# Kernel tuning notes

Hardware: AMD Instinct MI355X
Metric: run time of the kernel (lower is better)

The kernel has to match this reference:

```python
import jax, jax.numpy as jnp
import numpy as np

# ---- static config (matches init_kwargs: nlevs=[2,3,4], Pyr_mode=1, dfilt='pkva') ----
NLEVS = (2, 3, 4)
L = 3
# symmetric length-12 ladder (lifting) filter in the spirit of the 'pkva' ladder filter
_PKVA_HALF = np.array([0.6300, -0.1930, 0.0972, -0.0526, 0.0272, -0.0144])
PKVA = np.concatenate([_PKVA_HALF[::-1], _PKVA_HALF])


def _lp_hp_masks(H, W):
    """Meyer-style smooth lowpass/highpass frequency masks (rcos smooth_func)."""
    def phi(n):
        w = np.abs(2.0 * np.pi * np.fft.fftfreq(n))
        s = np.clip((w - np.pi / 3.0) / (np.pi / 3.0), 0.0, 1.0)
        beta = s ** 4 * (35.0 - 84.0 * s + 70.0 * s ** 2 - 20.0 * s ** 3)
        return np.cos(0.5 * np.pi * beta)
    Lm = phi(H)[:, None] * phi(W)[None, :]
    Hm = np.sqrt(np.clip(1.0 - Lm ** 2, 0.0, None))
    return jnp.asarray(Lm, jnp.float32), jnp.asarray(Hm, jnp.float32)


def _pyr_dec(x, nlev):
    """PyrNDDEC_mm, Pyr_mode=1: FFT-domain smooth LP/HP split, dyadic decimation of LP."""
    bands = []
    for _ in range(nlev):
        H, W = x.shape[-2], x.shape[-1]
        Lm, Hm = _lp_hp_masks(H, W)
        Xf = jnp.fft.fft2(x)
        bands.append(jnp.fft.ifft2(Xf * Hm).real.astype(x.dtype))
        x = jnp.fft.ifft2(Xf * Lm).real.astype(x.dtype)[..., ::2, ::2]
    return [x] + bands[::-1]  # y[0]=coarsest lowpass, y[1..L]=bandpass coarse->fine


def _conv1d_wrap(x, f, axis):
    """1D circular ('wrap') convolution along `axis`."""
    K = f.shape[0]
    x = jnp.moveaxis(x, axis, -1)
    pad = [(0, 0)] * (x.ndim - 1) + [(K // 2, K - 1 - K // 2)]
    xp = jnp.pad(x, pad, mode='wrap')
    shp = xp.shape
    y = jax.lax.conv_general_dilated(xp.reshape(-1, 1, shp[-1]),
                                     f.reshape(1, 1, K).astype(x.dtype), (1,), 'VALID')
    y = y.reshape(shp[:-1] + (shp[-1] - K + 1,))
    return jnp.moveaxis(y, -1, axis)


def _fan_split(x, axis, f):
    """One ladder-structured fan filter-bank stage with quincunx coset split."""
    other = -2 if axis == -1 else -1
    n_other = x.shape[other]
    shape = [1] * x.ndim
    shape[other] = n_other
    idx = jnp.arange(n_other)
    # fan <-> diamond modulation along the other axis
    sign = (1 - 2 * (idx % 2)).astype(x.dtype).reshape(shape)
    xm = x * sign
    # quincunx cosets: shift odd lines by 1 along split axis, then deinterleave
    parity = ((idx % 2) == 1).reshape(shape)
    xs = jnp.where(parity, jnp.roll(xm, -1, axis=axis), xm)
    if axis == -1:
        p0, p1 = xs[..., 0::2], xs[..., 1::2]
    else:
        p0, p1 = xs[..., 0::2, :], xs[..., 1::2, :]
    # ladder (lifting) predict/update with 1D filter f
    d = p1 - _conv1d_wrap(p0, f, axis)
    s = p0 + 0.5 * _conv1d_wrap(d, f, axis)
    return s, d


def _dfbdec(x, f, n):
    """n-level directional filter bank (ladder structure). Returns (2^n, ...) stack."""
    subs = x[None]  # (M, B, 1, H, W), all subbands same shape per level -> vectorized
    axis = -1
    for _ in range(n):
        s, d = _fan_split(subs, axis, f)
        subs = jnp.concatenate([s, d], axis=0)
        axis = -2 if axis == -1 else -1
    return subs


def setup_inputs() -> dict:
    key = jax.random.key(0)
    x = jax.random.normal(key, (16, 1, 1024, 1024), dtype=jnp.float32)
    return {"x": x}


def reference(x):
    f = jnp.asarray(PKVA, x.dtype)
    y = _pyr_dec(x, L)
    outs = [y[0]]  # coarsest lowpass (B,1,128,128)
    for k in range(1, L + 1):
        outs.append(_dfbdec(y[k], f, NLEVS[k - 1]))
    # (lowpass, 4 dirs @128x128, 8 dirs @(256,128), 16 dirs @(256,256))
    return tuple(outs)
```

## Files before the change

### kernel.cpp

```cpp
#include <hip/hip_runtime.h>
#include <math.h>

#define PI_F 3.14159265358979323846f

__constant__ float c_pkva[12] = {
  -0.0144f, 0.0272f, -0.0526f, 0.0972f, -0.193f, 0.63f,
   0.63f, -0.193f, 0.0972f, -0.0526f, 0.0272f, -0.0144f
};

constexpr int ilog2c(int n) { int l = 0; while (n > 1) { n >>= 1; ++l; } return l; }

__device__ float g_phi[1920];
__device__ float2 g_tw[512];
constexpr int phi_off(int N) {
  return (N == 1024) ? 0 : (N == 512) ? 1024 : (N == 256) ? 1536 : 1792;
}

__device__ __forceinline__ float phi_dev(int k, int n) {
  int kk = (k < n - k) ? k : (n - k);
  float w = 2.0f * PI_F * (float)kk / (float)n;
  float s = (w - PI_F / 3.0f) * (3.0f / PI_F);
  s = fminf(fmaxf(s, 0.0f), 1.0f);
  float s2 = s * s;
  float beta = s2 * s2 * (35.0f - 84.0f * s + 70.0f * s2 - 20.0f * s2 * s);
  return __cosf(0.5f * PI_F * beta);
}

__global__ void phi_init_k() {
  int i = blockIdx.x * 256 + threadIdx.x;
  if (i < 1024)      g_phi[i] = phi_dev(i, 1024);
  else if (i < 1536) g_phi[i] = phi_dev(i - 1024, 512);
  else if (i < 1792) g_phi[i] = phi_dev(i - 1536, 256);
  else if (i < 1920) g_phi[i] = phi_dev(i - 1792, 128);
  else {
    int idx = i - 1920;
    if (idx >= 1 && idx < 512) {
      int l = 31 - __clz(idx);
      int Ns = 1 << l;
      float th = 2.0f * PI_F * (float)(idx - Ns) / (float)(4 * Ns);
      g_tw[idx] = make_float2(cosf(th), sinf(th));
    }
  }
}

__device__ __forceinline__ float2 cmul(float2 a, float2 b) {
  return make_float2(a.x * b.x - a.y * b.y, a.x * b.y + a.y * b.x);
}
__device__ __forceinline__ float2 cadd(float2 a, float2 b) { return make_float2(a.x + b.x, a.y + b.y); }
__device__ __forceinline__ float2 csub(float2 a, float2 b) { return make_float2(a.x - b.x, a.y - b.y); }

template <int N>
__device__ __forceinline__ int fft_core4(float2 (*sbuf)[N], float dirsign, int tid, int cur) {
  constexpr int LOG2 = ilog2c(N);
  constexpr int NT = N / 4;
  constexpr bool LEAD2 = (LOG2 & 1);
  if constexpr (LEAD2) {
#pragma unroll
    for (int j = tid; j < N / 2; j += NT) {
      float2 v0 = sbuf[cur][j], v1 = sbuf[cur][j + N / 2];
      float2 e = cadd(v0, v1), o = csub(v0, v1);
      *(float4*)&sbuf[cur ^ 1][2 * j] = make_float4(e.x, e.y, o.x, o.y);
    }
    cur ^= 1;
    __syncthreads();
  }
#pragma unroll
  for (int Ns = LEAD2 ? 2 : 1; Ns < N; Ns <<= 2) {
    int j = tid;
    int base = j & (Ns - 1);
    float2 t = g_tw[Ns + base];
    float2 w1 = make_float2(t.x, dirsign * t.y);
    float2 w2 = cmul(w1, w1);
    float2 w3 = cmul(w2, w1);
    float2 v0 = sbuf[cur][j];
    float2 v1 = cmul(sbuf[cur][j + N / 4], w1);
    float2 v2 = cmul(sbuf[cur][j + N / 2], w2);
    float2 v3 = cmul(sbuf[cur][j + 3 * (N / 4)], w3);
    float2 a0 = cadd(v0, v2), a1 = csub(v0, v2);
    float2 a2 = cadd(v1, v3), a3 = csub(v1, v3);
    float2 r1 = make_float2(-dirsign * a3.y, dirsign * a3.x);
    int idxD = ((j - base) << 2) + base;
    cur ^= 1;
    sbuf[cur][idxD]          = cadd(a0, a2);
    sbuf[cur][idxD + Ns]     = cadd(a1, r1);
    sbuf[cur][idxD + 2 * Ns] = csub(a0, a2);
    sbuf[cur][idxD + 3 * Ns] = csub(a1, r1);
    __syncthreads();
  }
  return cur;
}

template <int N, int LMODE, int SMODE>
__global__ void __launch_bounds__(N / 4)
fft_rows_k(const void* __restrict__ vin, void* __restrict__ vout,
           float dirsign, float scale) {
  constexpr int NT = N / 4;
  __shared__ __align__(16) float2 sbuf[2][N];
  const int tid = threadIdx.x;
  const int row = blockIdx.x;
  const int r = row & (N - 1);

  if (LMODE == 1) {
    const float2* in = (const float2*)vin;
#pragma unroll
    for (int i = tid; i < N; i += NT) {
      float2 v = in[(size_t)row * N + i];
      sbuf[0][i] = make_float2(v.x * scale, v.y * scale);
    }
  } else {
    const float2* in = (const float2*)vin;
    float pr = g_phi[phi_off(N) + r];
#pragma unroll
    for (int i = tid; i < N; i += NT) {
      float lm = pr * g_phi[phi_off(N) + i];
      float m = sqrtf(fmaxf(1.0f - lm * lm, 0.0f)) * scale;
      float2 v = in[(size_t)row * N + i];
      sbuf[0][i] = make_float2(v.x * m, v.y * m);
    }
  }
  __syncthreads();

  int cur = fft_core4<N>(sbuf, dirsign, tid, 0);

  if (SMODE == 0) {
    float2* outp = (float2*)vout;
#pragma unroll
    for (int i = tid; i < N; i += NT)
      outp[(size_t)row * N + i] = sbuf[cur][i];
  } else {
    float* outp = (float*)vout;
#pragma unroll
    for (int i = tid; i < N; i += NT)
      outp[(size_t)row * N + i] = sbuf[cur][i].x;
  }
}

template <int N, int LMODE>
__global__ void __launch_bounds__(N / 4)
fft_rows_cm_k(const float2* __restrict__ in, float2* __restrict__ outcm,
              float scale) {
  constexpr int NT = N / 4;
  __shared__ __align__(16) float2 sbuf[2][N];
  const int tid = threadIdx.x;
  const int img = blockIdx.y;
  const int b = blockIdx.x;
  const int q = ((b & 7) << (ilog2c(N) - 4)) + (b >> 3);
  float2 r0v[4], r1v[4];

#pragma unroll
  for (int half = 0; half < 2; ++half) {
    const int r = 2 * q + half;
    if constexpr (LMODE == 1) {
      const float2* rp = in + ((size_t)img * N + r) * N;
#pragma unroll
      for (int i = tid; i < N; i += NT) {
        float2 v = rp[i];
        sbuf[0][i] = make_float2(v.x * scale, v.y * scale);
      }
    } else if constexpr (LMODE == 2) {
      const float2* rp = in + ((size_t)img * N + r) * N;
      float pr = g_phi[phi_off(N) + r];
#pragma unroll
      for (int i = tid; i < N; i += NT) {
        float lm = pr * g_phi[phi_off(N) + i];
        float m = sqrtf(fmaxf(1.0f - lm * lm, 0.0f)) * scale;
        float2 v = rp[i];
        sbuf[0][i] = make_float2(v.x * m, v.y * m);
      }
    } else {
      const float2* fb = in + (size_t)img * (513 * 512);
      const float2* fr0 = fb + (size_t)r * 512;
      const float2* fr1 = fb + (size_t)(512 - r) * 512;
      float pr = g_phi[phi_off(512) + r];
#pragma unroll
      for (int i = tid; i < N; i += NT) {
        float2 a = fr0[i], bb = fr1[(512 - i) & 511];
        float lm = pr * g_phi[phi_off(512) + i];
        float m = sqrtf(fmaxf(1.0f - lm * lm, 0.0f)) * scale;
        sbuf[0][i] = make_float2((a.x + bb.x) * m, (a.y - bb.y) * m);
      }
    }
    __syncthreads();

    int cur = fft_core4<N>(sbuf, 1.0f, tid, 0);

#pragma unroll
    for (int i = tid, k = 0; i < N; i += NT, ++k) {
      float2 v = sbuf[cur][i];
      if (half == 0) r0v[k] = v; else r1v[k] = v;
    }
    __syncthreads();
  }

  float2* ob = outcm + (size_t)img * N * N + 2 * q;
#pragma unroll
  for (int i = tid, k = 0; i < N; i += NT, ++k)
    *(float4*)&ob[(size_t)i * N] = make_float4(r0v[k].x, r0v[k].y, r1v[k].x, r1v[k].y);
}

template <int N, int PITCH>
__global__ void __launch_bounds__(N / 4)
rfft_pairs_cm_k(const float* __restrict__ in, float2* __restrict__ out) {
  constexpr int NT = N / 4;
  __shared__ __align__(16) float2 sbuf[2][N];
  const int tid = threadIdx.x;
  const int img = blockIdx.x >> (ilog2c(N) - 1);
  const int b = blockIdx.x & (N / 2 - 1);
  const int r = ((b & 7) << (ilog2c(N) - 4)) + (b >> 3);
  const float* p0 = in + ((size_t)img * N + 2 * r) * N;
  const float* p1 = p0 + N;

#pragma unroll
  for (int i = tid; i < N; i += NT)
    sbuf[0][i] = make_float2(p0[i], p1[i]);
  __syncthreads();

  int cur = fft_core4<N>(sbuf, -1.0f, tid, 0);

  float2* ob = out + (size_t)img * ((size_t)PITCH * N) + 2 * r;
#pragma unroll
  for (int i = tid; i <= N / 2; i += NT) {
    float2 Z = sbuf[cur][i];
    float2 Zr = sbuf[cur][(N - i) & (N - 1)];
    float2 Zc = make_float2(Zr.x, -Zr.y);
    float2 o0 = make_float2(0.5f * (Z.x + Zc.x), 0.5f * (Z.y + Zc.y));
    float2 dd = make_float2(Z.x - Zc.x, Z.y - Zc.y);
    float2 o1 = make_float2(0.5f * dd.y, -0.5f * dd.x);
    *(float4*)&ob[(size_t)i * N] = make_float4(o0.x, o0.y, o1.x, o1.y);
  }
}

__global__ void transpose_rect_k(const float2* __restrict__ in,
                                 float2* __restrict__ out, int R, int C) {
  __shared__ float2 tile[32][33];
  int img = blockIdx.z;
  size_t base = (size_t)img * R * C;
  int c = blockIdx.x * 32 + threadIdx.x;
  int r0 = blockIdx.y * 32;
  for (int j = threadIdx.y; j < 32; j += 8)
    tile[j][threadIdx.x] = in[base + (size_t)(r0 + j) * C + c];
  __syncthreads();
  int r = blockIdx.y * 32 + threadIdx.x;
  int c0 = blockIdx.x * 32;
  for (int j = threadIdx.y; j < 32; j += 8)
    out[base + (size_t)(c0 + j) * R + r] = tile[threadIdx.x][j];
}

template <int N, int PITCH>
__global__ void __launch_bounds__(N / 4)
fft_col_half_k(float2* __restrict__ inout, float2* __restrict__ foldb) {
  constexpr int NT = N / 4;
  constexpr int NH = N / 2;
  __shared__ __align__(16) float2 sbuf[2][N];
  const int tid = threadIdx.x;
  const int kx = blockIdx.x;
  const int img = blockIdx.y;
  float2* rowp = inout + ((size_t)img * PITCH + kx) * N;

#pragma unroll
  for (int i = tid; i < N; i += NT)
    sbuf[0][i] = rowp[i];
  __syncthreads();

  int cur = fft_core4<N>(sbuf, -1.0f, tid, 0);

  const float pr = g_phi[phi_off(N) + kx];
  const float inv = 1.0f / (float)N;
  float2* fp = foldb + ((size_t)img * (NH + 1) + kx) * NH;
#pragma unroll
  for (int i = tid; i < NH; i += NT) {
    float2 vA = sbuf[cur][i];
    float2 vB = sbuf[cur][i + NH];
    float lmA = pr * g_phi[phi_off(N) + i];
    float lmB = pr * g_phi[phi_off(N) + i + NH];
    fp[i] = make_float2(0.25f * (vA.x * lmA + vB.x * lmB),
                        0.25f * (vA.y * lmA + vB.y * lmB));
    float hmA = sqrtf(fmaxf(1.0f - lmA * lmA, 0.0f)) * inv;
    float hmB = sqrtf(fmaxf(1.0f - lmB * lmB, 0.0f)) * inv;
    sbuf[cur][i]      = make_float2(vA.x * hmA, vA.y * hmA);
    sbuf[cur][i + NH] = make_float2(vB.x * hmB, vB.y * hmB);
  }
  __syncthreads();

  cur = fft_core4<N>(sbuf, 1.0f, tid, cur);

#pragma unroll
  for (int i = tid; i < N; i += NT)
    rowp[i] = sbuf[cur][i];
}

__global__ void __launch_bounds__(256)
fold_spec3_k(const float2* __restrict__ fold, float2* __restrict__ spec3) {
  __shared__ float2 s2a[512], s2b[512];
  const int rp = blockIdx.x;
  const int img = blockIdx.y;
  const float2* fb = fold + (size_t)img * (513 * 512);
  const float2* fr0 = fb + (size_t)rp * 512;
  const float2* fr1 = fb + (size_t)(512 - rp) * 512;
  const float2* fr2 = fb + (size_t)(rp + 256) * 512;
  const float2* fr3 = fb + (size_t)(256 - rp) * 512;
  for (int c = threadIdx.x; c < 512; c += 256) {
    int mc = (512 - c) & 511;
    float2 a0 = fr0[c], b0 = fr1[mc];
    float2 a1 = fr2[c], b1 = fr3[mc];
    s2a[c] = make_float2(a0.x + b0.x, a0.y - b0.y);
    s2b[c] = make_float2(a1.x + b1.x, a1.y - b1.y);
  }
  __syncthreads();
  float pr0 = g_phi[phi_off(512) + rp], pr1 = g_phi[phi_off(512) + rp + 256];
  float2* sp3 = spec3 + ((size_t)img << 16) + ((size_t)rp << 8);
  {
    int c = threadIdx.x;
    float pc0 = g_phi[phi_off(512) + c], pc1 = g_phi[phi_off(512) + c + 256];
    float2 v00 = s2a[c], v01 = s2a[c + 256], v10 = s2b[c], v11 = s2b[c + 256];
    float m00 = pr0 * pc0, m01 = pr0 * pc1, m10 = pr1 * pc0, m11 = pr1 * pc1;
    sp3[c] = make_float2(
        0.25f * (v00.x * m00 + v01.x * m01 + v10.x * m10 + v11.x * m11),
        0.25f * (v00.y * m00 + v01.y * m01 + v10.y * m10 + v11.y * m11));
  }
}

template <int N, int PITCH>
__global__ void __launch_bounds__(N / 4)
ifft_fan_pair_k(const float2* __restrict__ in, float* __restrict__ outb,
                float scale, int halfT) {
  constexpr int NT = N / 4;
  constexpr int W2 = N / 2;
  __shared__ __align__(16) float2 sbuf[2][N];
  const int tid = threadIdx.x;
  const int img = blockIdx.x >> (ilog2c(N) - 1);
  const int q = blockIdx.x & (N / 2 - 1);
  const int y0 = 2 * q;
  const float2* inA = in + ((size_t)img * N + y0) * PITCH;
  const float2* inB = inA + PITCH;

#pragma unroll
  for (int i = tid; i <= W2; i += NT) {
    float2 a = inA[i], b = inB[i];
    sbuf[0][i] = make_float2((a.x - b.y) * scale, (a.y + b.x) * scale);
  }
#pragma unroll
  for (int i = tid; i < W2 - 1; i += NT) {
    int m = W2 - 1 - i;
    float2 a = inA[m], b = inB[m];
    sbuf[0][W2 + 1 + i] = make_float2((a.x + b.y) * scale, (b.x - a.y) * scale);
  }
  __syncthreads();

  int cur = fft_core4<N>(sbuf, 1.0f, tid, 0);

  float* scratch = (float*)sbuf[cur ^ 1];
  float* xe = scratch;
  float* xo = scratch + W2;
  float* db = scratch + 2 * W2;
  const size_t rbase = ((size_t)img * N + y0) * W2;

  for (int sub = 0; sub < 2; ++sub) {
    const int par = sub;
    const float sgn = par ? -1.0f : 1.0f;
#pragma unroll
    for (int i = tid; i < N; i += NT) {
      float v = par ? sbuf[cur][i].y : sbuf[cur][i].x;
      int ii = (i - par) & (N - 1);
      if (ii & 1) xo[ii >> 1] = v; else xe[ii >> 1] = v;
    }
    __syncthreads();

    float* outs = outb + rbase + (size_t)sub * W2;
    float* outd = outb + halfT + rbase + (size_t)sub * W2;
#pragma unroll 2
    for (int j = tid; j < W2; j += NT) {
      float acc = 0.0f;
#pragma unroll
      for (int k = 0; k < 12; k++)
        acc += c_pkva[k] * xe[(j - 6 + k + W2) & (W2 - 1)];
      float dv = sgn * (xo[j] - acc);
      db[j] = dv;
      outd[j] = dv;
    }
    __syncthreads();
#pragma unroll 2
    for (int j = tid; j < W2; j += NT) {
      float acc = 0.0f;
#pragma unroll
      for (int k = 0; k < 12; k++)
        acc += c_pkva[k] * db[(j - 6 + k + W2) & (W2 - 1)];
      outs[j] = sgn * xe[j] + 0.5f * acc;
    }
    __syncthreads();
  }
}

template <int N>
__global__ void __launch_bounds__(N / 4)
ifft_fan_k(const float2* __restrict__ in, float* __restrict__ outb,
           float scale, int halfT) {
  constexpr int NT = N / 4;
  constexpr int W2 = N / 2;
  __shared__ __align__(16) float2 sbuf[2][N];
  const int tid = threadIdx.x;
  const int nr = blockIdx.x;
  const int r = nr & (N - 1);
  const int par = r & 1;
  const float sgn = par ? -1.0f : 1.0f;

#pragma unroll
  for (int i = tid; i < N; i += NT) {
    float2 v = in[(size_t)nr * N + i];
    sbuf[0][i] = make_float2(v.x * scale, v.y * scale);
  }
  __syncthreads();

  int cur = fft_core4<N>(sbuf, 1.0f, tid, 0);

  float* scratch = (float*)sbuf[cur ^ 1];
  float* xe = scratch;
  float* xo = scratch + W2;
  float* db = scratch + 2 * W2;
#pragma unroll
  for (int i = tid; i < N; i += NT) {
    float v = sbuf[cur][i].x;
    int ii = (i - par) & (N - 1);
    if (ii & 1) xo[ii >> 1] = v; else xe[ii >> 1] = v;
  }
  __syncthreads();

  float* outs = outb + (size_t)nr * W2;
  float* outd = outb + halfT + (size_t)nr * W2;
#pragma unroll 2
  for (int j = tid; j < W2; j += NT) {
    float acc = 0.0f;
#pragma unroll
    for (int k = 0; k < 12; k++)
      acc += c_pkva[k] * xe[(j - 6 + k + W2) & (W2 - 1)];
    float dv = sgn * (xo[j] - acc);
    db[j] = dv;
    outd[j] = dv;
  }
  __syncthreads();
#pragma unroll 2
  for (int j = tid; j < W2; j += NT) {
    float acc = 0.0f;
#pragma unroll
    for (int k = 0; k < 12; k++)
      acc += c_pkva[k] * db[(j - 6 + k + W2) & (W2 - 1)];
    outs[j] = sgn * xe[j] + 0.5f * acc;
  }
}

__global__ void alias_k(const float2* __restrict__ in, float2* __restrict__ out,
                        int N, int lgN2, int phiOff) {
  int idx = blockIdx.x * 256 + threadIdx.x;
  int N2 = N >> 1;
  int c = idx & (N2 - 1);
  int r = (idx >> lgN2) & (N2 - 1);
  int img = idx >> (2 * lgN2);
  float pr0 = g_phi[phiOff + r], pr1 = g_phi[phiOff + r + N2];
  float pc0 = g_phi[phiOff + c], pc1 = g_phi[phiOff + c + N2];
  size_t base = (size_t)img * N * N;
  float2 v00 = in[base + (size_t)r * N + c];
  float2 v01 = in[base + (size_t)r * N + c + N2];
  float2 v10 = in[base + (size_t)(r + N2) * N + c];
  float2 v11 = in[base + (size_t)(r + N2) * N + c + N2];
  float m00 = pr0 * pc0, m01 = pr0 * pc1, m10 = pr1 * pc0, m11 = pr1 * pc1;
  float2 o;
  o.x = 0.25f * (v00.x * m00 + v01.x * m01 + v10.x * m10 + v11.x * m11);
  o.y = 0.25f * (v00.y * m00 + v01.y * m01 + v10.y * m10 + v11.y * m11);
  out[((size_t)img << (2 * lgN2)) + ((size_t)r << lgN2) + c] = o;
}

__global__ void __launch_bounds__(256)
fs_row_k(const float* __restrict__ x, float* __restrict__ outb,
         int lgH, int lgW, int halfT) {
  __shared__ float xe[512], xo[512], db[512];
  int H = 1 << lgH, W = 1 << lgW, W2 = W >> 1;
  int nr = blockIdx.x;
  int r = nr & (H - 1);
  int par = r & 1;
  float sgn = par ? -1.0f : 1.0f;
  const float* xrow = x + (size_t)nr * W;
  for (int j = threadIdx.x; j < W2; j += 256) {
    xe[j] = sgn * xrow[(2 * j + par) & (W - 1)];
    xo[j] = sgn * xrow[(2 * j + 1 + par) & (W - 1)];
  }
  __syncthreads();
  float* outs = outb + (size_t)nr * W2;
  float* outd = outb + halfT + (size_t)nr * W2;
  for (int j = threadIdx.x; j < W2; j += 256) {
    float acc = 0.0f;
#pragma unroll
    for (int k = 0; k < 12; k++)
      acc += c_pkva[k] * xe[(j - 6 + k + W2) & (W2 - 1)];
    float dv = xo[j] - acc;
    db[j] = dv;
    outd[j] = dv;
  }
  __syncthreads();
  for (int j = threadIdx.x; j < W2; j += 256) {
    float acc = 0.0f;
#pragma unroll
    for (int k = 0; k < 12; k++)
      acc += c_pkva[k] * db[(j - 6 + k + W2) & (W2 - 1)];
    outs[j] = xe[j] + 0.5f * acc;
  }
}

template <int TI, int TC>
__global__ void __launch_bounds__(256)
fs_col_fused_k(const float* __restrict__ x, float* __restrict__ outb,
               int lgH, int lgW, int halfT) {
  constexpr int RE = 2 * TI + 48;
  constexpr int DE = TI + 12;
  constexpr int NR = 256 / TC;
  __shared__ float raw[RE][TC];
  __shared__ float dvs[DE][TC];
  const int H = 1 << lgH, W = 1 << lgW;
  const int c0 = blockIdx.x * TC;
  const int i0 = blockIdx.y * TI;
  const int n = blockIdx.z;
  const int tc = threadIdx.x & (TC - 1);
  const int tr = threadIdx.x / TC;
  const float* xim = x + ((size_t)n << (lgH + lgW));
  const int rbase = 2 * i0 - 24;
#pragma unroll
  for (int r = tr; r < RE; r += NR) {
    int rr = (rbase + r) & (H - 1);
    raw[r][tc] = xim[((size_t)rr << lgW) + c0 + tc];
  }
  __syncthreads();
  const int par = tc & 1;
  for (int j = tr; j < DE; j += NR) {
    float acc = 0.0f;
#pragma unroll
    for (int k = 0; k < 12; k++)
      acc += c_pkva[k] * raw[2 * j + 2 * k + par][tc];
    dvs[j][tc] = raw[2 * j + 13 + par][tc] - acc;
  }
  __syncthreads();
  const float sgn = par ? -1.0f : 1.0f;
  float* outs = outb + (((size_t)n << (lgH - 1)) << lgW);
  float* outd = outs + halfT;
  for (int i = tr; i < TI; i += NR) {
    float acc = 0.0f;
#pragma unroll
    for (int k = 0; k < 12; k++)
      acc += c_pkva[k] * dvs[i + k][tc];
    float p0v = raw[2 * i + 24 + par][tc];
    size_t off = ((size_t)(i0 + i) << lgW) + c0 + tc;
    outd[off] = sgn * dvs[i + 6][tc];
    outs[off] = sgn * (p0v + 0.5f * acc);
  }
}

__global__ void fill_err_k(float* out) {
  out[threadIdx.x] = 1.0e9f;
}

extern "C" void kernel_launch(void* const* d_in, const int* in_sizes, int n_in,
                              void* d_out, int out_size, void* d_ws, size_t ws_size,
                              hipStream_t stream) {
  const float* x = (const float*)d_in[0];
  float* out = (float*)d_out;
  char* ws = (char*)d_ws;

  const size_t NEED = 220266496ull;
  if (ws_size < NEED) {
    fill_err_k<<<dim3(1), dim3(256), 0, stream>>>(out);
    return;
  }

  float2* bufA  = (float2*)(ws);
  float2* bufB  = (float2*)(ws + 71303168);
  float2* foldb = (float2*)(ws + 142606336);
  float2* spec3 = (float2*)(ws + 209780736);
  float2* spec4 = (float2*)(ws + 218169344);

  float* out0 = out;
  float* out1 = out + 262144;
  float* out2 = out + 1310720;
  float* out3 = out + 5505024;

  phi_init_k<<<dim3(10), dim3(256), 0, stream>>>();

  rfft_pairs_cm_k<1024, 544><<<dim3(8192), dim3(256), 0, stream>>>(x, bufB);
  fft_col_half_k<1024, 544><<<dim3(513, 16), dim3(256), 0, stream>>>(bufB, foldb);
  fold_spec3_k<<<dim3(256, 16), dim3(256), 0, stream>>>(foldb, spec3);
  transpose_rect_k<<<dim3(32, 17, 16), dim3(32, 8), 0, stream>>>(bufB, bufA, 544, 1024);
  ifft_fan_pair_k<1024, 544><<<dim3(8192), dim3(256), 0, stream>>>(bufA, (float*)bufB, 1.0f / 1024.0f, 8388608);
  fs_col_fused_k<64, 32><<<dim3(16, 8, 32), dim3(256), 0, stream>>>((float*)bufB, (float*)bufA, 10, 9, 8388608);
  fs_row_k<<<dim3(32768), dim3(256), 0, stream>>>((float*)bufA, (float*)bufB, 9, 9, 8388608);
  fs_col_fused_k<64, 32><<<dim3(8, 4, 128), dim3(256), 0, stream>>>((float*)bufB, out3, 9, 8, 8388608);

  fft_rows_cm_k<512, 3><<<dim3(256, 16), dim3(128), 0, stream>>>(foldb, bufA, 1.0f / 512.0f);
  ifft_fan_k<512><<<dim3(8192), dim3(128), 0, stream>>>(bufA, (float*)bufB, 1.0f / 512.0f, 2097152);
  fs_col_fused_k<64, 32><<<dim3(8, 4, 32), dim3(256), 0, stream>>>((float*)bufB, (float*)bufA, 9, 8, 2097152);
  fs_row_k<<<dim3(16384), dim3(256), 0, stream>>>((float*)bufA, out2, 8, 8, 2097152);

  alias_k<<<dim3(1024), dim3(256), 0, stream>>>(spec3, spec4, 256, 7, phi_off(256));
  fft_rows_cm_k<256, 2><<<dim3(128, 16), dim3(64), 0, stream>>>(spec3, bufA, 1.0f / 256.0f);
  ifft_fan_k<256><<<dim3(4096), dim3(64), 0, stream>>>(bufA, (float*)bufB, 1.0f / 256.0f, 524288);
  fs_col_fused_k<64, 32><<<dim3(4, 2, 32), dim3(256), 0, stream>>>((float*)bufB, out1, 8, 7, 524288);

  fft_rows_cm_k<128, 1><<<dim3(64, 16), dim3(32), 0, stream>>>(spec4, bufA, 1.0f / 128.0f);
  fft_rows_k<128, 1, 1><<<dim3(2048), dim3(32), 0, stream>>>((const void*)bufA, (void*)out0, 1.0f, 1.0f / 128.0f);
}
```

Baseline: 482.1 us.

## Fuse column FFT with transpose by processing row pairs and writing transposed output

```diff
diff --git a/kernel.cpp b/kernel.cpp
--- a/kernel.cpp
+++ b/kernel.cpp
@@ -185,17 +185,23 @@
     int cur = fft_core4<N>(sbuf, 1.0f, tid, 0);
 
 #pragma unroll
-    for (int i = tid, k = 0; i < N; i += NT, ++k) {
-      float2 v = sbuf[cur][i];
-      if (half == 0) r0v[k] = v; else r1v[k] = v;
+    for (int k = 0; k < 4; ++k) {
+      int i = tid + k * NT;
+      if (i < N) {
+        float2 v = sbuf[cur][i];
+        if (half == 0) r0v[k] = v; else r1v[k] = v;
+      }
     }
     __syncthreads();
   }
 
   float2* ob = outcm + (size_t)img * N * N + 2 * q;
 #pragma unroll
-  for (int i = tid, k = 0; i < N; i += NT, ++k)
-    *(float4*)&ob[(size_t)i * N] = make_float4(r0v[k].x, r0v[k].y, r1v[k].x, r1v[k].y);
+  for (int k = 0; k < 4; ++k) {
+    int i = tid + k * NT;
+    if (i < N)
+      *(float4*)&ob[(size_t)i * N] = make_float4(r0v[k].x, r0v[k].y, r1v[k].x, r1v[k].y);
+  }
 }
 
 template <int N, int PITCH>
@@ -230,63 +236,75 @@
   }
 }
 
-__global__ void transpose_rect_k(const float2* __restrict__ in,
-                                 float2* __restrict__ out, int R, int C) {
-  __shared__ float2 tile[32][33];
-  int img = blockIdx.z;
-  size_t base = (size_t)img * R * C;
-  int c = blockIdx.x * 32 + threadIdx.x;
-  int r0 = blockIdx.y * 32;
-  for (int j = threadIdx.y; j < 32; j += 8)
-    tile[j][threadIdx.x] = in[base + (size_t)(r0 + j) * C + c];
-  __syncthreads();
-  int r = blockIdx.y * 32 + threadIdx.x;
-  int c0 = blockIdx.x * 32;
-  for (int j = threadIdx.y; j < 32; j += 8)
-    out[base + (size_t)(c0 + j) * R + r] = tile[threadIdx.x][j];
-}
-
 template <int N, int PITCH>
 __global__ void __launch_bounds__(N / 4)
-fft_col_half_k(float2* __restrict__ inout, float2* __restrict__ foldb) {
+fft_col_half_pair_k(const float2* __restrict__ in, float2* __restrict__ outT,
+                    float2* __restrict__ foldb) {
   constexpr int NT = N / 4;
   constexpr int NH = N / 2;
+  constexpr int NP = N / 4;
   __shared__ __align__(16) float2 sbuf[2][N];
   const int tid = threadIdx.x;
-  const int kx = blockIdx.x;
   const int img = blockIdx.y;
-  float2* rowp = inout + ((size_t)img * PITCH + kx) * N;
-
-#pragma unroll
-  for (int i = tid; i < N; i += NT)
-    sbuf[0][i] = rowp[i];
-  __syncthreads();
-
-  int cur = fft_core4<N>(sbuf, -1.0f, tid, 0);
-
-  const float pr = g_phi[phi_off(N) + kx];
+  const int b = blockIdx.x;
+  const int t = (b < NP) ? (((b & 7) * (NP / 8)) + (b >> 3)) : NP;
   const float inv = 1.0f / (float)N;
-  float2* fp = foldb + ((size_t)img * (NH + 1) + kx) * NH;
-#pragma unroll
-  for (int i = tid; i < NH; i += NT) {
-    float2 vA = sbuf[cur][i];
-    float2 vB = sbuf[cur][i + NH];
-    float lmA = pr * g_phi[phi_off(N) + i];
-    float lmB = pr * g_phi[phi_off(N) + i + NH];
-    fp[i] = make_float2(0.25f * (vA.x * lmA + vB.x * lmB),
-                        0.25f * (vA.y * lmA + vB.y * lmB));
-    float hmA = sqrtf(fmaxf(1.0f - lmA * lmA, 0.0f)) * inv;
-    float hmB = sqrtf(fmaxf(1.0f - lmB * lmB, 0.0f)) * inv;
-    sbuf[cur][i]      = make_float2(vA.x * hmA, vA.y * hmA);
-    sbuf[cur][i + NH] = make_float2(vB.x * hmB, vB.y * hmB);
-  }
-  __syncthreads();
-
-  cur = fft_core4<N>(sbuf, 1.0f, tid, cur);
-
-#pragma unroll
-  for (int i = tid; i < N; i += NT)
-    rowp[i] = sbuf[cur][i];
+  float2 k0[4], k1[4];
+
+#pragma unroll 1
+  for (int half = 0; half < 2; ++half) {
+    const int kx = 2 * t + half;
+    if (kx > NH) break;
+    const float2* rowp = in + ((size_t)img * PITCH + kx) * N;
+#pragma unroll
+    for (int i = tid; i < N; i += NT)
+      sbuf[0][i] = rowp[i];
+    __syncthreads();
+
+    int cur = fft_core4<N>(sbuf, -1.0f, tid, 0);
+
+    const float pr = g_phi[phi_off(N) + kx];
+    float2* fp = foldb + ((size_t)img * (NH + 1) + kx) * NH;
+#pragma unroll
+    for (int i = tid; i < NH; i += NT) {
+      float2 vA = sbuf[cur][i];
+      float2 vB = sbuf[cur][i + NH];
+      float lmA = pr * g_phi[phi_off(N) + i];
+      float lmB = pr * g_phi[phi_off(N) + i + NH];
+      fp[i] = make_float2(0.25f * (vA.x * lmA + vB.x * lmB),
+                          0.25f * (vA.y * lmA + vB.y * lmB));
+      float hmA = sqrtf(fmaxf(1.0f - lmA * lmA, 0.0f)) * inv;
+      float hmB = sqrtf(fmaxf(1.0f - lmB * lmB, 0.0f)) * inv;
+      sbuf[cur][i]      = make_float2(vA.x * hmA, vA.y * hmA);
+      sbuf[cur][i + NH] = make_float2(vB.x * hmB, vB.y * hmB);
+    }
+    __syncthreads();
+
+    cur = fft_core4<N>(sbuf, 1.0f, tid, cur);
+
+#pragma unroll
+    for (int k = 0; k < 4; ++k) {
+      int i = tid + k * NT;
+      float2 v = sbuf[cur][i];
+      if (half == 0) k0[k] = v; else k1[k] = v;
+    }
+    __syncthreads();
+  }
+
+  if (t < NP) {
+#pragma unroll
+    for (int k = 0; k < 4; ++k) {
+      int i = tid + k * NT;
+      *(float4*)&outT[((size_t)img * N + i) * PITCH + 2 * t] =
+          make_float4(k0[k].x, k0[k].y, k1[k].x, k1[k].y);
+    }
+  } else {
+#pragma unroll
+    for (int k = 0; k < 4; ++k) {
+      int i = tid + k * NT;
+      outT[((size_t)img * N + i) * PITCH + NH] = k0[k];
+    }
+  }
 }
 
 __global__ void __launch_bounds__(256)
@@ -583,9 +601,8 @@
   phi_init_k<<<dim3(10), dim3(256), 0, stream>>>();
 
   rfft_pairs_cm_k<1024, 544><<<dim3(8192), dim3(256), 0, stream>>>(x, bufB);
-  fft_col_half_k<1024, 544><<<dim3(513, 16), dim3(256), 0, stream>>>(bufB, foldb);
+  fft_col_half_pair_k<1024, 544><<<dim3(257, 16), dim3(256), 0, stream>>>(bufB, bufA, foldb);
   fold_spec3_k<<<dim3(256, 16), dim3(256), 0, stream>>>(foldb, spec3);
-  transpose_rect_k<<<dim3(32, 17, 16), dim3(32, 8), 0, stream>>>(bufB, bufA, 544, 1024);
   ifft_fan_pair_k<1024, 544><<<dim3(8192), dim3(256), 0, stream>>>(bufA, (float*)bufB, 1.0f / 1024.0f, 8388608);
   fs_col_fused_k<64, 32><<<dim3(16, 8, 32), dim3(256), 0, stream>>>((float*)bufB, (float*)bufA, 10, 9, 8388608);
   fs_row_k<<<dim3(32768), dim3(256), 0, stream>>>((float*)bufA, (float*)bufB, 9, 9, 8388608);
```

After: 470.5 us. 2.4% less time.
